# Kernel optimization log

Hardware: AMD Instinct MI355X
Metric: run time of the kernel (lower is better)

Reference implementation:

```python
import jax, jax.numpy as jnp
import numpy as np
import itertools

LN_EPS = 1e-3  # keras LayerNormalization default epsilon

def _pair_indices(field_num):
    pairs = np.array(list(itertools.combinations(range(field_num), 2)), dtype=np.int32)
    return pairs[:, 0], pairs[:, 1]

def setup_inputs() -> dict:
    key = jax.random.key(0)
    ks = jax.random.split(key, 3)
    B, F, E, P, D = 2048, 40, 32, 780, 16
    x = jax.random.normal(ks[0], (B, F, E), dtype=jnp.float32)
    # glorot-normal-ish scaling for the bilinear pair weights
    W = jax.random.normal(ks[1], (P, E, E), dtype=jnp.float32) * (2.0 / (E + E)) ** 0.5
    dense_w = jax.random.normal(ks[2], (P, D), dtype=jnp.float32) * (2.0 / (P + D)) ** 0.5
    dense_b = jnp.zeros((D,), dtype=jnp.float32)
    gamma = jnp.ones((D,), dtype=jnp.float32)
    beta = jnp.zeros((D,), dtype=jnp.float32)
    return {"x": x, "W": W, "dense_w": dense_w, "dense_b": dense_b,
            "gamma": gamma, "beta": beta}

def reference(x, W, dense_w, dense_b, gamma, beta):
    F = x.shape[1]
    idx_i, idx_j = _pair_indices(F)           # static pair lists, P = C(F,2)
    xi = x[:, idx_i, :]                        # [B, P, E]
    xj = x[:, idx_j, :]                        # [B, P, E]
    # (x_i @ W_p) . x_j per pair, fused: p[b,p] = sum_ef xi[b,p,e] W[p,e,f] xj[b,p,f]
    t = jnp.einsum('bpe,pef->bpf', xi, W)      # [B, P, E]
    p = jnp.einsum('bpf,bpf->bp', t, xj)       # [B, P]
    # reducing layer: Dense(output_dim) + LayerNorm (no activation)
    h = p @ dense_w + dense_b                  # [B, D]
    mu = jnp.mean(h, axis=-1, keepdims=True)
    var = jnp.mean(jnp.square(h - mu), axis=-1, keepdims=True)
    out = (h - mu) * jax.lax.rsqrt(var + LN_EPS) * gamma + beta
    return out
```

## Files before the change

kernel.cpp:

```cpp
#include <hip/hip_runtime.h>
#include <hip/hip_bf16.h>

typedef __attribute__((ext_vector_type(8))) short bf16x8;
typedef __attribute__((ext_vector_type(4))) float f32x4;

#define B_NUM 2048
#define F_NUM 40
#define E_DIM 32
#define P_NUM 780
#define D_DIM 16
#define PC_N  78
#define PC_SZ 10
#define LN_EPS 1e-3f

#define WF_OFF 0
#define WF_BYTES (P_NUM * 2 * 64 * 8 * 2)
#define XB_OFF  WF_BYTES
#define XB_BYTES (F_NUM * 4 * B_NUM * 8 * 2)
#define DW_OFF  (XB_OFF + XB_BYTES)
#define DW_BYTES (P_NUM * D_DIM * 2)
#define HP_OFF  (DW_OFF + DW_BYTES)

static __device__ __forceinline__ unsigned short f2b(float f) {
  unsigned u = __builtin_bit_cast(unsigned, f);
  u += 0x7fffu + ((u >> 16) & 1u);
  return (unsigned short)(u >> 16);
}
static __device__ __forceinline__ short f2bs(float f) { return (short)f2b(f); }
static __device__ __forceinline__ short fcvt(float f) {
  return (short)__bfloat16_as_ushort(__float2bfloat16(f));
}
static __device__ __forceinline__ float b2f(unsigned short u) {
  return __builtin_bit_cast(float, (unsigned)u << 16);
}

__global__ __launch_bounds__(256) void prep_kernel(
    const float* __restrict__ x, const float* __restrict__ W,
    const float* __restrict__ dw, short* __restrict__ xbp,
    short* __restrict__ wfrag, unsigned short* __restrict__ dwbf) {
  const int lane = threadIdx.x & 63;
  const int wv   = threadIdx.x >> 6;
  const int lhi = lane >> 4, llo = lane & 15;
  __shared__ float wst[4][E_DIM * E_DIM];

  if (blockIdx.x < 640) {
    const int u  = blockIdx.x * 256 + threadIdx.x;
    const int b  = u & (B_NUM - 1);
    const int fp = u >> 11;
    const int f  = fp >> 1;
    const float* src = x + ((size_t)b * F_NUM + f) * E_DIM + (fp & 1) * 16;
    const float4 v0 = *reinterpret_cast<const float4*>(src);
    const float4 v1 = *reinterpret_cast<const float4*>(src + 4);
    const float4 v2 = *reinterpret_cast<const float4*>(src + 8);
    const float4 v3 = *reinterpret_cast<const float4*>(src + 12);
    const int plane = f * 4 + (fp & 1) * 2;
    bf16x8 o0, o1;
    o0[0] = f2bs(v0.x); o0[1] = f2bs(v0.y); o0[2] = f2bs(v0.z); o0[3] = f2bs(v0.w);
    o0[4] = f2bs(v1.x); o0[5] = f2bs(v1.y); o0[6] = f2bs(v1.z); o0[7] = f2bs(v1.w);
    o1[0] = f2bs(v2.x); o1[1] = f2bs(v2.y); o1[2] = f2bs(v2.z); o1[3] = f2bs(v2.w);
    o1[4] = f2bs(v3.x); o1[5] = f2bs(v3.y); o1[6] = f2bs(v3.z); o1[7] = f2bs(v3.w);
    *reinterpret_cast<bf16x8*>(xbp + ((size_t)plane * B_NUM + b) * 8)       = o0;
    *reinterpret_cast<bf16x8*>(xbp + ((size_t)(plane + 1) * B_NUM + b) * 8) = o1;
  } else if (blockIdx.x < 640 + 195) {
    const int p = (blockIdx.x - 640) * 4 + wv;
    const float* Wp = W + (size_t)p * (E_DIM * E_DIM);
#pragma unroll
    for (int k = 0; k < 4; ++k) {
      float4 v = *reinterpret_cast<const float4*>(Wp + k * 256 + lane * 4);
      *reinterpret_cast<float4*>(&wst[wv][k * 256 + lane * 4]) = v;
    }
#pragma unroll
    for (int frag = 0; frag < 2; ++frag) {
      const int fo = (llo >> 2) * 8 + frag * 4 + (llo & 3);
      bf16x8 v;
#pragma unroll
      for (int t = 0; t < 8; ++t)
        v[t] = f2bs(wst[wv][(lhi * 8 + t) * E_DIM + fo]);
      *reinterpret_cast<bf16x8*>(wfrag + ((size_t)(p * 2 + frag) * 64 + lane) * 8) = v;
    }
  } else {
    for (int t = threadIdx.x; t < P_NUM * D_DIM; t += 256) dwbf[t] = f2b(dw[t]);
  }
}

__global__ __launch_bounds__(256, 4) void fused_bilinear_dense_kernel(
    const short* __restrict__ xbp, const short* __restrict__ wfrag,
    const unsigned short* __restrict__ dwbf, float* __restrict__ hpart) {
  const int lane = threadIdx.x & 63;
  const int wv   = threadIdx.x >> 6;
  const int lhi = lane >> 4, llo = lane & 15;
  const int bb = blockIdx.x * 128 + wv * 32;
  const int pc = blockIdx.y;
  const int p0 = pc * PC_SZ;

  const int off0 = (lhi * B_NUM + bb + llo) * 8;
  const int off1 = off0 + 16 * 8;
#define XB8(f, o) (*reinterpret_cast<const bf16x8*>(xbp + (size_t)(f) * 65536 + (o)))
#define AFR(p, fr) (*reinterpret_cast<const bf16x8*>( \
    wfrag + ((size_t)((p) * 2 + (fr)) * 64 + lane) * 8))

  int ii[PC_SZ], jj[PC_SZ];
  {
    int i = 0;
    while ((i + 1) * (79 - (i + 1)) / 2 <= p0) ++i;
    ii[0] = i; jj[0] = i + 1 + (p0 - i * (79 - i) / 2);
  }
#pragma unroll
  for (int k = 1; k < PC_SZ; ++k) {
    int in_ = ii[k - 1], jn = jj[k - 1] + 1;
    if (jn == F_NUM) { ++in_; jn = in_ + 1; }
    ii[k] = in_; jj[k] = jn;
  }

  bf16x8 sa0[2], sa1[2], sxj0[2], sxj1[2], sbf0[2], sbf1[2];
  unsigned short sdw[2];
#pragma unroll
  for (int k = 0; k < 2; ++k) {
    sa0[k] = AFR(p0 + k, 0);  sa1[k] = AFR(p0 + k, 1);
    sxj0[k] = XB8(jj[k], off0); sxj1[k] = XB8(jj[k], off1);
    sbf0[k] = XB8(ii[k], off0); sbf1[k] = XB8(ii[k], off1);
    sdw[k] = dwbf[(p0 + k) * D_DIM + llo];
  }

  f32x4 acc0 = {0.f, 0.f, 0.f, 0.f};
  f32x4 acc1 = {0.f, 0.f, 0.f, 0.f};
  const f32x4 z = {0.f, 0.f, 0.f, 0.f};

#pragma unroll
  for (int k = 0; k < PC_SZ; ++k) {
    const int s = k & 1;
    const bf16x8 a0 = sa0[s], a1 = sa1[s];
    const bf16x8 xj0 = sxj0[s], xj1 = sxj1[s];
    const bf16x8 bf0 = sbf0[s], bf1 = sbf1[s];
    const unsigned short dwb = sdw[s];
    if (k + 2 < PC_SZ) {
      sa0[s] = AFR(p0 + k + 2, 0);  sa1[s] = AFR(p0 + k + 2, 1);
      sxj0[s] = XB8(jj[k + 2], off0); sxj1[s] = XB8(jj[k + 2], off1);
      sbf0[s] = XB8(ii[k + 2], off0); sbf1[s] = XB8(ii[k + 2], off1);
      sdw[s] = dwbf[(p0 + k + 2) * D_DIM + llo];
    }

    const f32x4 c00 = __builtin_amdgcn_mfma_f32_16x16x32_bf16(a0, bf0, z, 0, 0, 0);
    const f32x4 c01 = __builtin_amdgcn_mfma_f32_16x16x32_bf16(a1, bf0, z, 0, 0, 0);
    const f32x4 c10 = __builtin_amdgcn_mfma_f32_16x16x32_bf16(a0, bf1, z, 0, 0, 0);
    const f32x4 c11 = __builtin_amdgcn_mfma_f32_16x16x32_bf16(a1, bf1, z, 0, 0, 0);

    bf16x8 a2;
#pragma unroll
    for (int t = 0; t < 8; ++t) a2[t] = (short)dwb;

    bf16x8 u0, u1;
#pragma unroll
    for (int t = 0; t < 4; ++t) {
      u0[t]     = fcvt(c00[t] * b2f((unsigned short)xj0[t]));
      u0[t + 4] = fcvt(c01[t] * b2f((unsigned short)xj0[t + 4]));
      u1[t]     = fcvt(c10[t] * b2f((unsigned short)xj1[t]));
      u1[t + 4] = fcvt(c11[t] * b2f((unsigned short)xj1[t + 4]));
    }

    acc0 = __builtin_amdgcn_mfma_f32_16x16x32_bf16(a2, u0, acc0, 0, 0, 0);
    acc1 = __builtin_amdgcn_mfma_f32_16x16x32_bf16(a2, u1, acc1, 0, 0, 0);
  }
#undef XB8
#undef AFR

  float* hp = hpart + (size_t)pc * B_NUM * D_DIM;
  *reinterpret_cast<f32x4*>(hp + (size_t)(bb + llo) * D_DIM + lhi * 4) = acc0;
  *reinterpret_cast<f32x4*>(hp + (size_t)(bb + 16 + llo) * D_DIM + lhi * 4) = acc1;
}

__global__ __launch_bounds__(256) void reduce_ln_kernel(
    const float* __restrict__ hpart, const float* __restrict__ bias,
    const float* __restrict__ gamma, const float* __restrict__ beta,
    float* __restrict__ out) {
  const int t = threadIdx.x;
  const int d = t & 15;
  const int b = blockIdx.x * 16 + (t >> 4);
  float acc = bias[d];
  const float* hp = hpart + (size_t)b * D_DIM + d;
#pragma unroll 6
  for (int pc = 0; pc < PC_N; ++pc)
    acc += hp[(size_t)pc * B_NUM * D_DIM];

  float sum = acc;
  sum += __shfl_xor(sum, 1); sum += __shfl_xor(sum, 2);
  sum += __shfl_xor(sum, 4); sum += __shfl_xor(sum, 8);
  const float mu = sum * (1.f / D_DIM);
  const float dev = acc - mu;
  float v = dev * dev;
  v += __shfl_xor(v, 1); v += __shfl_xor(v, 2);
  v += __shfl_xor(v, 4); v += __shfl_xor(v, 8);
  const float rs = rsqrtf(v * (1.f / D_DIM) + LN_EPS);
  out[(size_t)b * D_DIM + d] = dev * rs * gamma[d] + beta[d];
}

extern "C" void kernel_launch(void* const* d_in, const int* in_sizes, int n_in,
                              void* d_out, int out_size, void* d_ws, size_t ws_size,
                              hipStream_t stream) {
  const float* x     = (const float*)d_in[0];
  const float* W     = (const float*)d_in[1];
  const float* dw    = (const float*)d_in[2];
  const float* db    = (const float*)d_in[3];
  const float* gamma = (const float*)d_in[4];
  const float* beta  = (const float*)d_in[5];
  float* out = (float*)d_out;

  short*          wfrag = (short*)((char*)d_ws + WF_OFF);
  short*          xbp   = (short*)((char*)d_ws + XB_OFF);
  unsigned short* dwbf  = (unsigned short*)((char*)d_ws + DW_OFF);
  float*          hpart = (float*)((char*)d_ws + HP_OFF);

  prep_kernel<<<640 + 195 + 1, 256, 0, stream>>>(x, W, dw, xbp, wfrag, dwbf);

  dim3 gA(B_NUM / 128, PC_N);
  fused_bilinear_dense_kernel<<<gA, 256, 0, stream>>>(xbp, wfrag, dwbf, hpart);

  reduce_ln_kernel<<<B_NUM / 16, 256, 0, stream>>>(hpart, db, gamma, beta, out);
}
```

Before: 35.94 us.

## Shrink pair chunks, single-buffer prefetch, reuse xi loads, raise occupancy

The pair-chunk size drops from 10 to 6, so the grid grows to 130 chunks. The main kernel moves from a two-deep register prefetch to a one-deep one, skips reloading x_i when the row index is unchanged, and raises launch bounds to 8 waves per SIMD, aiming at more parallelism and occupancy. The reduce kernel now uses 128-thread blocks. In exchange there are more partial-sum slices to write and reduce (130 instead of 78), which adds hpart traffic, and the shallower prefetch hides less latency.

Result: slower. 41.23 us (+14.7%).

```diff
diff --git a/kernel.cpp b/kernel.cpp
--- a/kernel.cpp
+++ b/kernel.cpp
@@ -9,8 +9,8 @@
 #define E_DIM 32
 #define P_NUM 780
 #define D_DIM 16
-#define PC_N  78
-#define PC_SZ 10
+#define PC_N  130
+#define PC_SZ 6
 #define LN_EPS 1e-3f
 
 #define WF_OFF 0
@@ -83,7 +83,7 @@
   }
 }
 
-__global__ __launch_bounds__(256, 4) void fused_bilinear_dense_kernel(
+__global__ __launch_bounds__(256, 8) void fused_bilinear_dense_kernel(
     const short* __restrict__ xbp, const short* __restrict__ wfrag,
     const unsigned short* __restrict__ dwbf, float* __restrict__ hpart) {
   const int lane = threadIdx.x & 63;
@@ -112,15 +112,10 @@
     ii[k] = in_; jj[k] = jn;
   }
 
-  bf16x8 sa0[2], sa1[2], sxj0[2], sxj1[2], sbf0[2], sbf1[2];
-  unsigned short sdw[2];
-#pragma unroll
-  for (int k = 0; k < 2; ++k) {
-    sa0[k] = AFR(p0 + k, 0);  sa1[k] = AFR(p0 + k, 1);
-    sxj0[k] = XB8(jj[k], off0); sxj1[k] = XB8(jj[k], off1);
-    sbf0[k] = XB8(ii[k], off0); sbf1[k] = XB8(ii[k], off1);
-    sdw[k] = dwbf[(p0 + k) * D_DIM + llo];
-  }
+  bf16x8 bf0 = XB8(ii[0], off0), bf1 = XB8(ii[0], off1);
+  bf16x8 xj0 = XB8(jj[0], off0), xj1 = XB8(jj[0], off1);
+  bf16x8 a0 = AFR(p0, 0), a1 = AFR(p0, 1);
+  unsigned short dwb = dwbf[p0 * D_DIM + llo];
 
   f32x4 acc0 = {0.f, 0.f, 0.f, 0.f};
   f32x4 acc1 = {0.f, 0.f, 0.f, 0.f};
@@ -128,18 +123,16 @@
 
 #pragma unroll
   for (int k = 0; k < PC_SZ; ++k) {
-    const int s = k & 1;
-    const bf16x8 a0 = sa0[s], a1 = sa1[s];
-    const bf16x8 xj0 = sxj0[s], xj1 = sxj1[s];
-    const bf16x8 bf0 = sbf0[s], bf1 = sbf1[s];
-    const unsigned short dwb = sdw[s];
-    if (k + 2 < PC_SZ) {
-      sa0[s] = AFR(p0 + k + 2, 0);  sa1[s] = AFR(p0 + k + 2, 1);
-      sxj0[s] = XB8(jj[k + 2], off0); sxj1[s] = XB8(jj[k + 2], off1);
-      sbf0[s] = XB8(ii[k + 2], off0); sbf1[s] = XB8(ii[k + 2], off1);
-      sdw[s] = dwbf[(p0 + k + 2) * D_DIM + llo];
-    }
-
+    bf16x8 nxj0 = xj0, nxj1 = xj1, na0 = a0, na1 = a1, nbf0 = bf0, nbf1 = bf1;
+    unsigned short ndw = dwb;
+    if (k + 1 < PC_SZ) {
+      nxj0 = XB8(jj[k + 1], off0); nxj1 = XB8(jj[k + 1], off1);
+      na0 = AFR(p0 + k + 1, 0);    na1 = AFR(p0 + k + 1, 1);
+      ndw = dwbf[(p0 + k + 1) * D_DIM + llo];
+      if (ii[k + 1] != ii[k]) {
+        nbf0 = XB8(ii[k + 1], off0); nbf1 = XB8(ii[k + 1], off1);
+      }
+    }
     const f32x4 c00 = __builtin_amdgcn_mfma_f32_16x16x32_bf16(a0, bf0, z, 0, 0, 0);
     const f32x4 c01 = __builtin_amdgcn_mfma_f32_16x16x32_bf16(a1, bf0, z, 0, 0, 0);
     const f32x4 c10 = __builtin_amdgcn_mfma_f32_16x16x32_bf16(a0, bf1, z, 0, 0, 0);
@@ -160,6 +153,9 @@
 
     acc0 = __builtin_amdgcn_mfma_f32_16x16x32_bf16(a2, u0, acc0, 0, 0, 0);
     acc1 = __builtin_amdgcn_mfma_f32_16x16x32_bf16(a2, u1, acc1, 0, 0, 0);
+
+    xj0 = nxj0; xj1 = nxj1; a0 = na0; a1 = na1; bf0 = nbf0; bf1 = nbf1;
+    dwb = ndw;
   }
 #undef XB8
 #undef AFR
@@ -169,16 +165,16 @@
   *reinterpret_cast<f32x4*>(hp + (size_t)(bb + 16 + llo) * D_DIM + lhi * 4) = acc1;
 }
 
-__global__ __launch_bounds__(256) void reduce_ln_kernel(
+__global__ __launch_bounds__(128) void reduce_ln_kernel(
     const float* __restrict__ hpart, const float* __restrict__ bias,
     const float* __restrict__ gamma, const float* __restrict__ beta,
     float* __restrict__ out) {
   const int t = threadIdx.x;
   const int d = t & 15;
-  const int b = blockIdx.x * 16 + (t >> 4);
+  const int b = blockIdx.x * 8 + (t >> 4);
   float acc = bias[d];
   const float* hp = hpart + (size_t)b * D_DIM + d;
-#pragma unroll 6
+#pragma unroll 5
   for (int pc = 0; pc < PC_N; ++pc)
     acc += hp[(size_t)pc * B_NUM * D_DIM];
 
@@ -215,5 +211,5 @@
   dim3 gA(B_NUM / 128, PC_N);
   fused_bilinear_dense_kernel<<<gA, 256, 0, stream>>>(xbp, wfrag, dwbf, hpart);
 
-  reduce_ln_kernel<<<B_NUM / 16, 256, 0, stream>>>(hpart, db, gamma, beta, out);
-}
+  reduce_ln_kernel<<<B_NUM / 8, 128, 0, stream>>>(hpart, db, gamma, beta, out);
+}
```

## Drop x bf16 pre-pass; stream fp32 x rows via async LDS loads

Applied to the files above, without the earlier changes.

Removes the prep stage that converted x into a bf16 planar layout. The main kernel now reads fp32 x directly. x_j slabs are staged into swizzled shared memory through global_load_lds with a triple-buffered pipeline and explicit vmcnt waits, and x_i is loaded and converted in registers only when the i index changes. Pair chunks per block are doubled, which halves the partial-sum buffer and the reduce work. In exchange the kernel reads fp32 x, twice the bytes, relies on hand-tuned wait counts, and drops the occupancy launch bound.

Result: slower. 38.38 us (+6.8%).

```diff
diff --git a/kernel.cpp b/kernel.cpp
--- a/kernel.cpp
+++ b/kernel.cpp
@@ -9,15 +9,14 @@
 #define E_DIM 32
 #define P_NUM 780
 #define D_DIM 16
-#define PC_N  78
-#define PC_SZ 10
+#define PC_N  39
+#define PC_SZ 20
+#define XROW  (F_NUM * E_DIM)
 #define LN_EPS 1e-3f
 
 #define WF_OFF 0
 #define WF_BYTES (P_NUM * 2 * 64 * 8 * 2)
-#define XB_OFF  WF_BYTES
-#define XB_BYTES (F_NUM * 4 * B_NUM * 8 * 2)
-#define DW_OFF  (XB_OFF + XB_BYTES)
+#define DW_OFF  WF_BYTES
 #define DW_BYTES (P_NUM * D_DIM * 2)
 #define HP_OFF  (DW_OFF + DW_BYTES)
 
@@ -30,39 +29,26 @@
 static __device__ __forceinline__ short fcvt(float f) {
   return (short)__bfloat16_as_ushort(__float2bfloat16(f));
 }
-static __device__ __forceinline__ float b2f(unsigned short u) {
-  return __builtin_bit_cast(float, (unsigned)u << 16);
+
+static __device__ __forceinline__ bf16x8 xi_bf(const float* p) {
+  float4 a = *reinterpret_cast<const float4*>(p);
+  float4 b = *reinterpret_cast<const float4*>(p + 4);
+  bf16x8 v;
+  v[0] = fcvt(a.x); v[1] = fcvt(a.y); v[2] = fcvt(a.z); v[3] = fcvt(a.w);
+  v[4] = fcvt(b.x); v[5] = fcvt(b.y); v[6] = fcvt(b.z); v[7] = fcvt(b.w);
+  return v;
 }
 
 __global__ __launch_bounds__(256) void prep_kernel(
-    const float* __restrict__ x, const float* __restrict__ W,
-    const float* __restrict__ dw, short* __restrict__ xbp,
+    const float* __restrict__ W, const float* __restrict__ dw,
     short* __restrict__ wfrag, unsigned short* __restrict__ dwbf) {
   const int lane = threadIdx.x & 63;
   const int wv   = threadIdx.x >> 6;
   const int lhi = lane >> 4, llo = lane & 15;
   __shared__ float wst[4][E_DIM * E_DIM];
 
-  if (blockIdx.x < 640) {
-    const int u  = blockIdx.x * 256 + threadIdx.x;
-    const int b  = u & (B_NUM - 1);
-    const int fp = u >> 11;
-    const int f  = fp >> 1;
-    const float* src = x + ((size_t)b * F_NUM + f) * E_DIM + (fp & 1) * 16;
-    const float4 v0 = *reinterpret_cast<const float4*>(src);
-    const float4 v1 = *reinterpret_cast<const float4*>(src + 4);
-    const float4 v2 = *reinterpret_cast<const float4*>(src + 8);
-    const float4 v3 = *reinterpret_cast<const float4*>(src + 12);
-    const int plane = f * 4 + (fp & 1) * 2;
-    bf16x8 o0, o1;
-    o0[0] = f2bs(v0.x); o0[1] = f2bs(v0.y); o0[2] = f2bs(v0.z); o0[3] = f2bs(v0.w);
-    o0[4] = f2bs(v1.x); o0[5] = f2bs(v1.y); o0[6] = f2bs(v1.z); o0[7] = f2bs(v1.w);
-    o1[0] = f2bs(v2.x); o1[1] = f2bs(v2.y); o1[2] = f2bs(v2.z); o1[3] = f2bs(v2.w);
-    o1[4] = f2bs(v3.x); o1[5] = f2bs(v3.y); o1[6] = f2bs(v3.z); o1[7] = f2bs(v3.w);
-    *reinterpret_cast<bf16x8*>(xbp + ((size_t)plane * B_NUM + b) * 8)       = o0;
-    *reinterpret_cast<bf16x8*>(xbp + ((size_t)(plane + 1) * B_NUM + b) * 8) = o1;
-  } else if (blockIdx.x < 640 + 195) {
-    const int p = (blockIdx.x - 640) * 4 + wv;
+  if (blockIdx.x < 195) {
+    const int p = blockIdx.x * 4 + wv;
     const float* Wp = W + (size_t)p * (E_DIM * E_DIM);
 #pragma unroll
     for (int k = 0; k < 4; ++k) {
@@ -83,9 +69,10 @@
   }
 }
 
-__global__ __launch_bounds__(256, 4) void fused_bilinear_dense_kernel(
-    const short* __restrict__ xbp, const short* __restrict__ wfrag,
+__global__ __launch_bounds__(256) void fused_bilinear_dense_kernel(
+    const float* __restrict__ x, const short* __restrict__ wfrag,
     const unsigned short* __restrict__ dwbf, float* __restrict__ hpart) {
+  __shared__ __align__(16) float slabs[4][3][1024];
   const int lane = threadIdx.x & 63;
   const int wv   = threadIdx.x >> 6;
   const int lhi = lane >> 4, llo = lane & 15;
@@ -93,11 +80,28 @@
   const int pc = blockIdx.y;
   const int p0 = pc * PC_SZ;
 
-  const int off0 = (lhi * B_NUM + bb + llo) * 8;
-  const int off1 = off0 + 16 * 8;
-#define XB8(f, o) (*reinterpret_cast<const bf16x8*>(xbp + (size_t)(f) * 65536 + (o)))
+  const float* xw = x + (size_t)bb * XROW;
+
+  const int sr = lane >> 3;
+  const int sc = lane & 7;
+  const int scs = sc ^ sr;
+
+#define STAGE(st, jcol) do {                                                   \
+    _Pragma("unroll")                                                          \
+    for (int q = 0; q < 4; ++q)                                                \
+      __builtin_amdgcn_global_load_lds(                                        \
+          xw + (size_t)(q * 8 + sr) * XROW + (jcol) * E_DIM + scs * 4,         \
+          &slabs[wv][st][q * 256], 16, 0, 0);                                  \
+  } while (0)
+
 #define AFR(p, fr) (*reinterpret_cast<const bf16x8*>( \
     wfrag + ((size_t)((p) * 2 + (fr)) * 64 + lane) * 8))
+
+  const int sw = llo & 7;
+  const int rb00 = llo * 128 + (((lhi * 2)     ^ sw) << 4);
+  const int rb01 = llo * 128 + (((lhi * 2 + 1) ^ sw) << 4);
+  const int rb10 = rb00 + 16 * 128;
+  const int rb11 = rb01 + 16 * 128;
 
   int ii[PC_SZ], jj[PC_SZ];
   {
@@ -112,15 +116,17 @@
     ii[k] = in_; jj[k] = jn;
   }
 
-  bf16x8 sa0[2], sa1[2], sxj0[2], sxj1[2], sbf0[2], sbf1[2];
-  unsigned short sdw[2];
-#pragma unroll
-  for (int k = 0; k < 2; ++k) {
-    sa0[k] = AFR(p0 + k, 0);  sa1[k] = AFR(p0 + k, 1);
-    sxj0[k] = XB8(jj[k], off0); sxj1[k] = XB8(jj[k], off1);
-    sbf0[k] = XB8(ii[k], off0); sbf1[k] = XB8(ii[k], off1);
-    sdw[k] = dwbf[(p0 + k) * D_DIM + llo];
-  }
+  unsigned short dwp[2];
+  dwp[0] = dwbf[p0 * D_DIM + llo];
+  dwp[1] = dwbf[(p0 + 1) * D_DIM + llo];
+  bf16x8 bf0 = xi_bf(xw + (size_t)llo * XROW + ii[0] * E_DIM + lhi * 8);
+  bf16x8 bf1 = xi_bf(xw + (size_t)(llo + 16) * XROW + ii[0] * E_DIM + lhi * 8);
+  STAGE(0, jj[0]);
+  STAGE(1, jj[1]);
+  STAGE(2, jj[2]);
+  bf16x8 af0[2], af1[2];
+  af0[0] = AFR(p0, 0);     af1[0] = AFR(p0, 1);
+  af0[1] = AFR(p0 + 1, 0); af1[1] = AFR(p0 + 1, 1);
 
   f32x4 acc0 = {0.f, 0.f, 0.f, 0.f};
   f32x4 acc1 = {0.f, 0.f, 0.f, 0.f};
@@ -128,18 +134,23 @@
 
 #pragma unroll
   for (int k = 0; k < PC_SZ; ++k) {
-    const int s = k & 1;
-    const bf16x8 a0 = sa0[s], a1 = sa1[s];
-    const bf16x8 xj0 = sxj0[s], xj1 = sxj1[s];
-    const bf16x8 bf0 = sbf0[s], bf1 = sbf1[s];
-    const unsigned short dwb = sdw[s];
-    if (k + 2 < PC_SZ) {
-      sa0[s] = AFR(p0 + k + 2, 0);  sa1[s] = AFR(p0 + k + 2, 1);
-      sxj0[s] = XB8(jj[k + 2], off0); sxj1[s] = XB8(jj[k + 2], off1);
-      sbf0[s] = XB8(ii[k + 2], off0); sbf1[s] = XB8(ii[k + 2], off1);
-      sdw[s] = dwbf[(p0 + k + 2) * D_DIM + llo];
-    }
-
+    if (k == 0)                asm volatile("s_waitcnt vmcnt(12)" ::: "memory");
+    else if (k < PC_SZ - 2)    asm volatile("s_waitcnt vmcnt(9)"  ::: "memory");
+    else if (k == PC_SZ - 2)   asm volatile("s_waitcnt vmcnt(6)"  ::: "memory");
+    else                       asm volatile("s_waitcnt vmcnt(0)"  ::: "memory");
+    __builtin_amdgcn_sched_barrier(0);
+
+    const char* sb = (const char*)&slabs[wv][k % 3][0];
+    const f32x4 xj0a = *reinterpret_cast<const f32x4*>(sb + rb00);
+    const f32x4 xj0b = *reinterpret_cast<const f32x4*>(sb + rb01);
+    const f32x4 xj1a = *reinterpret_cast<const f32x4*>(sb + rb10);
+    const f32x4 xj1b = *reinterpret_cast<const f32x4*>(sb + rb11);
+
+    asm volatile("s_waitcnt lgkmcnt(0)" ::: "memory");
+    __builtin_amdgcn_sched_barrier(0);
+    if (k + 3 < PC_SZ) STAGE((k + 3) % 3, jj[k + 3]);
+
+    const bf16x8 a0 = af0[k & 1], a1 = af1[k & 1];
     const f32x4 c00 = __builtin_amdgcn_mfma_f32_16x16x32_bf16(a0, bf0, z, 0, 0, 0);
     const f32x4 c01 = __builtin_amdgcn_mfma_f32_16x16x32_bf16(a1, bf0, z, 0, 0, 0);
     const f32x4 c10 = __builtin_amdgcn_mfma_f32_16x16x32_bf16(a0, bf1, z, 0, 0, 0);
@@ -147,21 +158,31 @@
 
     bf16x8 a2;
 #pragma unroll
-    for (int t = 0; t < 8; ++t) a2[t] = (short)dwb;
+    for (int t = 0; t < 8; ++t) a2[t] = (short)dwp[k & 1];
 
     bf16x8 u0, u1;
 #pragma unroll
     for (int t = 0; t < 4; ++t) {
-      u0[t]     = fcvt(c00[t] * b2f((unsigned short)xj0[t]));
-      u0[t + 4] = fcvt(c01[t] * b2f((unsigned short)xj0[t + 4]));
-      u1[t]     = fcvt(c10[t] * b2f((unsigned short)xj1[t]));
-      u1[t + 4] = fcvt(c11[t] * b2f((unsigned short)xj1[t + 4]));
+      u0[t]     = fcvt(c00[t] * xj0a[t]);
+      u0[t + 4] = fcvt(c01[t] * xj0b[t]);
+      u1[t]     = fcvt(c10[t] * xj1a[t]);
+      u1[t + 4] = fcvt(c11[t] * xj1b[t]);
     }
 
     acc0 = __builtin_amdgcn_mfma_f32_16x16x32_bf16(a2, u0, acc0, 0, 0, 0);
     acc1 = __builtin_amdgcn_mfma_f32_16x16x32_bf16(a2, u1, acc1, 0, 0, 0);
-  }
-#undef XB8
+
+    if (k + 2 < PC_SZ) {
+      af0[k & 1] = AFR(p0 + k + 2, 0);
+      af1[k & 1] = AFR(p0 + k + 2, 1);
+      dwp[k & 1] = dwbf[(p0 + k + 2) * D_DIM + llo];
+    }
+    if (k + 1 < PC_SZ && ii[k + 1] != ii[k]) {
+      bf0 = xi_bf(xw + (size_t)llo * XROW + ii[k + 1] * E_DIM + lhi * 8);
+      bf1 = xi_bf(xw + (size_t)(llo + 16) * XROW + ii[k + 1] * E_DIM + lhi * 8);
+    }
+  }
+#undef STAGE
 #undef AFR
 
   float* hp = hpart + (size_t)pc * B_NUM * D_DIM;
@@ -178,7 +199,7 @@
   const int b = blockIdx.x * 16 + (t >> 4);
   float acc = bias[d];
   const float* hp = hpart + (size_t)b * D_DIM + d;
-#pragma unroll 6
+#pragma unroll 3
   for (int pc = 0; pc < PC_N; ++pc)
     acc += hp[(size_t)pc * B_NUM * D_DIM];
 
@@ -206,14 +227,13 @@
   float* out = (float*)d_out;
 
   short*          wfrag = (short*)((char*)d_ws + WF_OFF);
-  short*          xbp   = (short*)((char*)d_ws + XB_OFF);
   unsigned short* dwbf  = (unsigned short*)((char*)d_ws + DW_OFF);
   float*          hpart = (float*)((char*)d_ws + HP_OFF);
 
-  prep_kernel<<<640 + 195 + 1, 256, 0, stream>>>(x, W, dw, xbp, wfrag, dwbf);
+  prep_kernel<<<196, 256, 0, stream>>>(W, dw, wfrag, dwbf);
 
   dim3 gA(B_NUM / 128, PC_N);
-  fused_bilinear_dense_kernel<<<gA, 256, 0, stream>>>(xbp, wfrag, dwbf, hpart);
+  fused_bilinear_dense_kernel<<<gA, 256, 0, stream>>>(x, wfrag, dwbf, hpart);
 
   reduce_ln_kernel<<<B_NUM / 16, 256, 0, stream>>>(hpart, db, gamma, beta, out);
 }
```
